# Kernel tuning notes

Measured on AMD Instinct MI355X. Metric: run time of the kernel, lower is better.

Reference implementation:

```python
import jax, jax.numpy as jnp
import numpy as np

A = 5.0  # smoothness parameter 'a'

def setup_inputs() -> dict:
    key = jax.random.key(0)
    kx, kw = jax.random.split(key)
    x = jax.random.uniform(kx, (1024, 512), dtype=jnp.float32)
    weight = jax.random.uniform(kw, (512, 512), dtype=jnp.float32)
    return {"x": x, "weight": weight}

def reference(x, weight):
    # inner: [batch, in, out] broadcast min
    inner = jnp.minimum(x[..., None], weight[None])
    # smooth union (smooth max) over the 'in' dim: logsumexp(a*z)/a
    smooth = jax.scipy.special.logsumexp(A * inner, axis=-2) / A
    hard = jnp.max(inner, axis=-2)
    # straight-through: forward value = hard, gradient flows through smooth
    return jax.lax.stop_gradient(hard - smooth) + smooth
```

## Files before the change

kernel.cpp:

```cpp
#include <hip/hip_runtime.h>


typedef _Float16 h2 __attribute__((ext_vector_type(2)));
typedef unsigned int uint32;

#define MDIM 1024
#define KDIM 512
#define NDIM 512
#define K2   (KDIM / 2)
#define MB   8
#define NT   256
#define NWAVE 8
#define KP   (K2 / NWAVE)

__device__ __forceinline__ h2 h2min(h2 a, h2 b) { return __builtin_elementwise_min(a, b); }
__device__ __forceinline__ h2 h2max(h2 a, h2 b) { return __builtin_elementwise_max(a, b); }

__global__ __launch_bounds__(512) void pack_f16(const float* __restrict__ x,
                                                const float* __restrict__ w,
                                                uint32* __restrict__ xp,
                                                uint32* __restrict__ wp)
{
    const int b = blockIdx.x, tid = threadIdx.x;
    if (b < 256) {
        const int idx = b * 512 + tid;
        const int k2 = idx >> 9, n = idx & 511;
        h2 v;
        v[0] = (_Float16)w[(size_t)(2 * k2) * NDIM + n];
        v[1] = (_Float16)w[(size_t)(2 * k2 + 1) * NDIM + n];
        wp[idx] = __builtin_bit_cast(uint32, v);
    } else {
        const int idx = (b - 256) * 512 + tid;
        const float2 f = ((const float2*)x)[idx];
        h2 v;
        v[0] = (_Float16)f.x;
        v[1] = (_Float16)f.y;
        xp[idx] = __builtin_bit_cast(uint32, v);
    }
}

__global__ __launch_bounds__(512, 2) void tropical_h16(
    const uint32* __restrict__ xp,
    const uint32* __restrict__ wp,
    float* __restrict__ out)
{
    const int tid  = threadIdx.x;
    const int lane = tid & 63;
    const int wv   = tid >> 6;
    const int m0   = blockIdx.x * MB;
    const int n0   = blockIdx.y * NT;
    const int kp0  = __builtin_amdgcn_readfirstlane(wv * KP);

    __shared__ float red[NWAVE][MB][NT];

    const uint4* __restrict__ wb =
        (const uint4*)(wp + (size_t)kp0 * NDIM + n0) + lane;
    const uint32* __restrict__ xr0 = xp + (size_t)m0 * K2 + kp0;

    h2 acc[MB][4];
#pragma unroll
    for (int r = 0; r < MB; ++r)
#pragma unroll
        for (int j = 0; j < 4; ++j) acc[r][j] = (h2)0;

    uint4 A = wb[0], B = wb[(size_t)128];

#pragma unroll 2
    for (int i = 0; i < KP; ++i) {
        uint4 C;
        if (i + 2 < KP) C = wb[(size_t)(i + 2) * 128];
#pragma unroll
        for (int r = 0; r < MB; ++r) {
            const h2 xv = __builtin_bit_cast(h2, xr0[(size_t)r * K2 + i]);
            acc[r][0] = h2max(acc[r][0], h2min(xv, __builtin_bit_cast(h2, A.x)));
            acc[r][1] = h2max(acc[r][1], h2min(xv, __builtin_bit_cast(h2, A.y)));
            acc[r][2] = h2max(acc[r][2], h2min(xv, __builtin_bit_cast(h2, A.z)));
            acc[r][3] = h2max(acc[r][3], h2min(xv, __builtin_bit_cast(h2, A.w)));
        }
        A = B; B = C;
    }

#pragma unroll
    for (int r = 0; r < MB; ++r) {
        float4 v;
        v.x = fmaxf((float)acc[r][0][0], (float)acc[r][0][1]);
        v.y = fmaxf((float)acc[r][1][0], (float)acc[r][1][1]);
        v.z = fmaxf((float)acc[r][2][0], (float)acc[r][2][1]);
        v.w = fmaxf((float)acc[r][3][0], (float)acc[r][3][1]);
        ((float4*)&red[wv][r][0])[lane] = v;
    }
    __syncthreads();

    {
        const int r  = tid >> 6;
        const int c4 = tid & 63;
        float4 v = ((const float4*)&red[0][r][0])[c4];
#pragma unroll
        for (int q = 1; q < NWAVE; ++q) {
            float4 u = ((const float4*)&red[q][r][0])[c4];
            v.x = fmaxf(v.x, u.x); v.y = fmaxf(v.y, u.y);
            v.z = fmaxf(v.z, u.z); v.w = fmaxf(v.w, u.w);
        }
        *(float4*)(out + (size_t)(m0 + r) * NDIM + n0 + 4 * c4) = v;
    }
}

extern "C" void kernel_launch(void* const* d_in, const int* in_sizes, int n_in,
                              void* d_out, int out_size, void* d_ws, size_t ws_size,
                              hipStream_t stream) {
    const float* x = (const float*)d_in[0];
    const float* w = (const float*)d_in[1];
    float* out = (float*)d_out;

    uint32* xp = (uint32*)d_ws;
    uint32* wp = xp + (size_t)MDIM * K2;

    pack_f16<<<dim3(768), dim3(512), 0, stream>>>(x, w, xp, wp);
    tropical_h16<<<dim3(MDIM / MB, NDIM / NT), dim3(512), 0, stream>>>(xp, wp, out);
}
```

Before: 74.02 us.

## Stage weights via direct global-to-LDS loads with double buffering, x tile in LDS

Replaces the per-wave register prefetch of packed weights with asynchronous global_load_lds transfers into a per-wave double buffer in shared memory, consumed in chunks of four k-pairs. The block's x tile is copied into LDS once up front instead of being read from global memory on every iteration. The aim is to hide global latency and cut redundant scalar x loads, at the cost of a larger LDS footprint (72KB), which may limit occupancy, and hand-coded waitcnt values.

```diff
diff --git a/kernel.cpp b/kernel.cpp
--- a/kernel.cpp
+++ b/kernel.cpp
@@ -7,14 +7,19 @@
 #define MDIM 1024
 #define KDIM 512
 #define NDIM 512
-#define K2   (KDIM / 2)
+#define K2   256
 #define MB   8
 #define NT   256
 #define NWAVE 8
-#define KP   (K2 / NWAVE)
+#define KP   32
+#define CH   4
+#define NCH  (KP / CH)
 
 __device__ __forceinline__ h2 h2min(h2 a, h2 b) { return __builtin_elementwise_min(a, b); }
 __device__ __forceinline__ h2 h2max(h2 a, h2 b) { return __builtin_elementwise_max(a, b); }
+
+typedef const __attribute__((address_space(1))) uint32 guint;
+typedef __attribute__((address_space(3))) uint32 luint;
 
 __global__ __launch_bounds__(512) void pack_f16(const float* __restrict__ x,
                                                 const float* __restrict__ w,
@@ -39,7 +44,7 @@
     }
 }
 
-__global__ __launch_bounds__(512, 2) void tropical_h16(
+__global__ __launch_bounds__(512, 2) void tropical_r15(
     const uint32* __restrict__ xp,
     const uint32* __restrict__ wp,
     float* __restrict__ out)
@@ -49,13 +54,29 @@
     const int wv   = tid >> 6;
     const int m0   = blockIdx.x * MB;
     const int n0   = blockIdx.y * NT;
-    const int kp0  = __builtin_amdgcn_readfirstlane(wv * KP);
+    const int kp0  = wv * KP;
 
-    __shared__ float red[NWAVE][MB][NT];
+    __shared__ uint32 smem[18432];
+    uint32* xs    = smem;
+    uint32* wbase = smem + 2048;
 
-    const uint4* __restrict__ wb =
-        (const uint4*)(wp + (size_t)kp0 * NDIM + n0) + lane;
-    const uint32* __restrict__ xr0 = xp + (size_t)m0 * K2 + kp0;
+    {
+        const uint4* src = (const uint4*)(xp + (size_t)m0 * K2);
+        ((uint4*)xs)[tid] = src[tid];
+    }
+    __syncthreads();
+
+    uint32* mybuf = wbase + wv * 2048;
+    const uint32* __restrict__ wsrc = wp + (size_t)kp0 * NDIM + n0;
+
+    auto stage = [&](int c) {
+        uint32* dst = mybuf + (c & 1) * 1024;
+        const uint32* g = wsrc + (size_t)c * CH * NDIM + lane * 4;
+#pragma unroll
+        for (int r = 0; r < CH; ++r)
+            __builtin_amdgcn_global_load_lds((guint*)(g + (size_t)r * NDIM),
+                                             (luint*)(dst + r * 256), 16, 0, 0);
+    };
 
     h2 acc[MB][4];
 #pragma unroll
@@ -63,23 +84,32 @@
 #pragma unroll
         for (int j = 0; j < 4; ++j) acc[r][j] = (h2)0;
 
-    uint4 A = wb[0], B = wb[(size_t)128];
-
-#pragma unroll 2
-    for (int i = 0; i < KP; ++i) {
-        uint4 C;
-        if (i + 2 < KP) C = wb[(size_t)(i + 2) * 128];
+    stage(0);
+    for (int c = 0; c < NCH; ++c) {
+        if (c + 1 < NCH) {
+            stage(c + 1);
+            __builtin_amdgcn_s_waitcnt(0x0F74);
+        } else {
+            __builtin_amdgcn_s_waitcnt(0x0F70);
+        }
+        const uint32* lw = mybuf + (c & 1) * 1024;
+        const uint32* xc = xs + kp0 + c * CH;
 #pragma unroll
-        for (int r = 0; r < MB; ++r) {
-            const h2 xv = __builtin_bit_cast(h2, xr0[(size_t)r * K2 + i]);
-            acc[r][0] = h2max(acc[r][0], h2min(xv, __builtin_bit_cast(h2, A.x)));
-            acc[r][1] = h2max(acc[r][1], h2min(xv, __builtin_bit_cast(h2, A.y)));
-            acc[r][2] = h2max(acc[r][2], h2min(xv, __builtin_bit_cast(h2, A.z)));
-            acc[r][3] = h2max(acc[r][3], h2min(xv, __builtin_bit_cast(h2, A.w)));
+        for (int j = 0; j < CH; ++j) {
+            const uint4 A = *(const uint4*)(lw + j * 256 + lane * 4);
+#pragma unroll
+            for (int r = 0; r < MB; ++r) {
+                const h2 xv = __builtin_bit_cast(h2, xc[r * 256 + j]);
+                acc[r][0] = h2max(acc[r][0], h2min(xv, __builtin_bit_cast(h2, A.x)));
+                acc[r][1] = h2max(acc[r][1], h2min(xv, __builtin_bit_cast(h2, A.y)));
+                acc[r][2] = h2max(acc[r][2], h2min(xv, __builtin_bit_cast(h2, A.z)));
+                acc[r][3] = h2max(acc[r][3], h2min(xv, __builtin_bit_cast(h2, A.w)));
+            }
         }
-        A = B; B = C;
     }
 
+    __syncthreads();
+    float* red = (float*)(smem + 2048);
 #pragma unroll
     for (int r = 0; r < MB; ++r) {
         float4 v;
@@ -87,17 +117,17 @@
         v.y = fmaxf((float)acc[r][1][0], (float)acc[r][1][1]);
         v.z = fmaxf((float)acc[r][2][0], (float)acc[r][2][1]);
         v.w = fmaxf((float)acc[r][3][0], (float)acc[r][3][1]);
-        ((float4*)&red[wv][r][0])[lane] = v;
+        ((float4*)(red + ((size_t)wv * MB + r) * NT))[lane] = v;
     }
     __syncthreads();
 
     {
         const int r  = tid >> 6;
         const int c4 = tid & 63;
-        float4 v = ((const float4*)&red[0][r][0])[c4];
+        float4 v = ((const float4*)(red + (size_t)r * NT))[c4];
 #pragma unroll
         for (int q = 1; q < NWAVE; ++q) {
-            float4 u = ((const float4*)&red[q][r][0])[c4];
+            float4 u = ((const float4*)(red + ((size_t)q * MB + r) * NT))[c4];
             v.x = fmaxf(v.x, u.x); v.y = fmaxf(v.y, u.y);
             v.z = fmaxf(v.z, u.z); v.w = fmaxf(v.w, u.w);
         }
@@ -116,5 +146,5 @@
     uint32* wp = xp + (size_t)MDIM * K2;
 
     pack_f16<<<dim3(768), dim3(512), 0, stream>>>(x, w, xp, wp);
-    tropical_h16<<<dim3(MDIM / MB, NDIM / NT), dim3(512), 0, stream>>>(xp, wp, out);
+    tropical_r15<<<dim3(MDIM / MB, NDIM / NT), dim3(512), 0, stream>>>(xp, wp, out);
 }
```

Result: faster. 72.33 us (-2.3%).
